# Kernel optimization log

Measured on AMD Instinct MI355X. Metric: run time of the kernel, lower is better.

Reference implementation:

```python
import jax, jax.numpy as jnp
import numpy as np

B, T, E = 64, 64, 256
S, ENC = 128, 1024
RNN, ATT, DENSE = 1024, 1024, 8000


def setup_inputs() -> dict:
    key = jax.random.key(0)
    ks = jax.random.split(key, 16)
    s = 0.02
    return {
        "initial_input": jax.random.normal(ks[0], (B, T, E), jnp.float32),
        "hidden": jax.random.normal(ks[1], (B, RNN), jnp.float32),
        "cell": jax.random.normal(ks[2], (B, RNN), jnp.float32),
        "encoder_output": jax.random.normal(ks[3], (B, S, ENC), jnp.float32),
        "W1": jax.random.normal(ks[4], (RNN, ATT), jnp.float32) * s,
        "b1": jnp.zeros((ATT,), jnp.float32),
        "W2": jax.random.normal(ks[5], (ENC, ATT), jnp.float32) * s,
        "b2": jnp.zeros((ATT,), jnp.float32),
        "V": jax.random.normal(ks[6], (ATT, 1), jnp.float32) * s,
        "bV": jnp.zeros((1,), jnp.float32),
        "kernel": jax.random.normal(ks[7], (ENC + E, 4 * RNN), jnp.float32) * s,
        "rkernel": jax.random.normal(ks[8], (RNN, 4 * RNN), jnp.float32) * s,
        "bias": jnp.zeros((4 * RNN,), jnp.float32),
        "Wd": jax.random.normal(ks[9], (RNN, DENSE), jnp.float32) * s,
        "bd": jnp.zeros((DENSE,), jnp.float32),
        "seq_len": T,
    }


def _decode(initial_input, hidden, cell, encoder_output,
            W1, b1, W2, b2, V, bV, kernel, rkernel, bias, Wd, bd):
    # Keys W2(encoder_output) are step-independent: precompute once. [B,S,ATT]
    keys = jnp.einsum('bse,ea->bsa', encoder_output, W2) + b2

    def step(carry, x_t):
        h, c = carry
        # Bahdanau attention: score = V^T tanh(W1 h + W2 enc)
        q = h @ W1 + b1                                  # [B,ATT]
        score = jnp.tanh(q[:, None, :] + keys) @ V + bV   # [B,S,1]
        attn = jax.nn.softmax(score, axis=1)              # [B,S,1]
        ctx = jnp.sum(attn * encoder_output, axis=1)      # [B,ENC]
        # LSTM cell (Keras gate order i,f,g,o; sigmoid/tanh activations)
        inp = jnp.concatenate([ctx, x_t], axis=-1)        # [B,ENC+E]
        z = inp @ kernel + h @ rkernel + bias              # [B,4*RNN]
        i, f, g, o = jnp.split(z, 4, axis=-1)
        i = jax.nn.sigmoid(i)
        f = jax.nn.sigmoid(f)
        g = jnp.tanh(g)
        o = jax.nn.sigmoid(o)
        c_new = f * c + i * g
        h_new = o * jnp.tanh(c_new)
        logits = h_new @ Wd + bd                           # [B,DENSE]
        return (h_new, c_new), logits

    xs = jnp.swapaxes(initial_input, 0, 1)  # [T,B,E]
    (h, c), logits = jax.lax.scan(step, (hidden, cell), xs)
    outputs = jnp.swapaxes(logits, 0, 1)    # [B,T,DENSE]
    return outputs, h, c


def reference(initial_input, hidden, cell, encoder_output,
              W1, b1, W2, b2, V, bV, kernel, rkernel, bias, Wd, bd, seq_len):
    # seq_len == initial_input.shape[1] (static); the Python loop in the
    # original is expressed as an efficient lax.scan over decode steps.
    return _decode(initial_input[:, :seq_len, :], hidden, cell, encoder_output,
                   W1, b1, W2, b2, V, bV, kernel, rkernel, bias, Wd, bd)
```

## Files before the change

kernel.cpp:

```cpp
#include <hip/hip_runtime.h>
#include <hip/hip_bf16.h>
#include <stdint.h>


typedef __attribute__((ext_vector_type(8))) short short8;
typedef __attribute__((ext_vector_type(4))) float floatx4;
typedef __attribute__((ext_vector_type(4))) unsigned short ushortx4;

__device__ __forceinline__ float b2f(unsigned short u) {
    union { unsigned int i; float f; } v; v.i = ((unsigned int)u) << 16; return v.f;
}
__device__ __forceinline__ unsigned short f2b(float f) {
    union { float f; unsigned int i; } v; v.f = f;
    unsigned int r = v.i + 0x7fffu + ((v.i >> 16) & 1u);
    return (unsigned short)(r >> 16);
}
__device__ __forceinline__ float ftanh(float x) {
    x = fminf(15.f, fmaxf(-15.f, x));
    float e = __expf(2.f * x);
    return (e - 1.f) * __builtin_amdgcn_rcpf(e + 1.f);
}
__device__ __forceinline__ float fsig(float x) {
    return __builtin_amdgcn_rcpf(1.f + __expf(-x));
}
__device__ __forceinline__ void ld_lds16(const void* g, void* l) {
    __builtin_amdgcn_global_load_lds((const __attribute__((address_space(1))) void*)g,
                                     (__attribute__((address_space(3))) void*)l, 16, 0, 0);
}

__global__ __launch_bounds__(256) void conv_f32_bf16(
    const float* __restrict__ src, unsigned short* __restrict__ dst, int n4)
{
    int i = blockIdx.x * 256 + threadIdx.x;
    if (i < n4) {
        float4 v = ((const float4*)src)[i];
        ushortx4 o;
        o[0] = f2b(v.x); o[1] = f2b(v.y); o[2] = f2b(v.z); o[3] = f2b(v.w);
        ((ushortx4*)dst)[i] = o;
    }
}

__global__ __launch_bounds__(256) void transpose_conv(
    const float* __restrict__ src, int srcld,
    unsigned short* __restrict__ dst, int dstld, int coloff, int perm)
{
    __shared__ float tile[32][33];
    const int k0 = blockIdx.y * 32, n0 = blockIdx.x * 32;
    const int r = threadIdx.x >> 3, c = (threadIdx.x & 7) * 4;
    int n = n0 + c;
    int cn = perm ? ((((n >> 4) & 3) << 10) | ((n >> 6) << 4) | (n & 15)) : n;
    float4 v = *(const float4*)&src[(size_t)(k0 + r) * srcld + cn];
    tile[r][c + 0] = v.x; tile[r][c + 1] = v.y;
    tile[r][c + 2] = v.z; tile[r][c + 3] = v.w;
    __syncthreads();
    const int nr = threadIdx.x >> 3, kc = (threadIdx.x & 7) * 4;
    ushortx4 o;
    o[0] = f2b(tile[kc + 0][nr]);
    o[1] = f2b(tile[kc + 1][nr]);
    o[2] = f2b(tile[kc + 2][nr]);
    o[3] = f2b(tile[kc + 3][nr]);
    *(ushortx4*)&dst[(size_t)(n0 + nr) * dstld + coloff + k0 + kc] = o;
}

__global__ __launch_bounds__(256) void gemm_bf16_128(
    const unsigned short* __restrict__ A, int lda,
    const unsigned short* __restrict__ BT, int ldbt, int K,
    float* __restrict__ Cf, unsigned short* __restrict__ Cb,
    int ldc, int ncols, const float* __restrict__ bias)
{
    __shared__ __align__(16) unsigned short As[128 * 32];
    __shared__ __align__(16) unsigned short Bs[128 * 32];
    const int tid = threadIdx.x, wave = tid >> 6, lane = tid & 63;
    const int q = lane >> 4, lm = lane & 15;
    const int wr = wave >> 1, wc = wave & 1;
    const int m0 = blockIdx.y * 128, n0 = blockIdx.x * 128;
    const int srow = lane >> 2;
    const int gch = (lane & 3) ^ ((lane >> 3) & 3);
    const unsigned short* Ag0 = A + (size_t)(m0 + wave * 32 + srow) * lda + gch * 8;
    const unsigned short* Ag1 = Ag0 + (size_t)16 * lda;
    const unsigned short* Bg0 = BT + (size_t)(n0 + wave * 32 + srow) * ldbt + gch * 8;
    const unsigned short* Bg1 = Bg0 + (size_t)16 * ldbt;
    unsigned short* Al0 = &As[(wave * 32) * 32];
    unsigned short* Al1 = &As[(wave * 32 + 16) * 32];
    unsigned short* Bl0 = &Bs[(wave * 32) * 32];
    unsigned short* Bl1 = &Bs[(wave * 32 + 16) * 32];

    const floatx4 z4 = {0.f, 0.f, 0.f, 0.f};
    floatx4 acc[4][4];
#pragma unroll
    for (int i = 0; i < 4; i++)
#pragma unroll
        for (int j = 0; j < 4; j++) acc[i][j] = z4;
    const int ach = ((q ^ ((lm >> 1) & 3))) * 8;

    for (int kb = 0; kb < K; kb += 32) {
        ld_lds16(Ag0 + kb, Al0);
        ld_lds16(Ag1 + kb, Al1);
        ld_lds16(Bg0 + kb, Bl0);
        ld_lds16(Bg1 + kb, Bl1);
        __syncthreads();
        short8 a[4], b[4];
#pragma unroll
        for (int i = 0; i < 4; i++) a[i] = *(const short8*)&As[(wr * 64 + i * 16 + lm) * 32 + ach];
#pragma unroll
        for (int j = 0; j < 4; j++) b[j] = *(const short8*)&Bs[(wc * 64 + j * 16 + lm) * 32 + ach];
#pragma unroll
        for (int i = 0; i < 4; i++)
#pragma unroll
            for (int j = 0; j < 4; j++)
                acc[i][j] = __builtin_amdgcn_mfma_f32_16x16x32_bf16(a[i], b[j], acc[i][j], 0, 0, 0);
        __syncthreads();
    }
    const int rb = m0 + wr * 64 + q * 4;
#pragma unroll
    for (int i = 0; i < 4; i++) {
#pragma unroll
        for (int j = 0; j < 4; j++) {
            int col = n0 + wc * 64 + j * 16 + lm;
            if (col < ncols) {
                float bv = bias ? bias[col] : 0.f;
#pragma unroll
                for (int r = 0; r < 4; r++) {
                    float v = acc[i][j][r] + bv;
                    size_t idx = (size_t)(rb + i * 16 + r) * ldc + col;
                    if (Cf) Cf[idx] = v;
                    if (Cb) Cb[idx] = f2b(v);
                }
            }
        }
    }
}

__global__ __launch_bounds__(256) void gemm64_split(
    const unsigned short* __restrict__ A, int lda,
    const unsigned short* __restrict__ BT, int ldbt,
    int kchunk, float* __restrict__ Cpart, int ldc)
{
    __shared__ __align__(16) unsigned short As[4][64 * 32];
    __shared__ __align__(16) unsigned short Bs[4][64 * 32];
    const int tid = threadIdx.x, wave = tid >> 6, lane = tid & 63;
    const int q = lane >> 4, lm = lane & 15;
    const int n0 = blockIdx.x * 64;
    const int k0 = blockIdx.z * kchunk;
    const int srow = lane >> 2;
    const int gch = (lane & 3) ^ ((lane >> 3) & 3);
    const unsigned short* Ag = A + (size_t)(wave * 16 + srow) * lda + k0 + gch * 8;
    const unsigned short* Bg = BT + (size_t)(n0 + wave * 16 + srow) * ldbt + k0 + gch * 8;
    const int loff = (wave * 16) * 32;
    const floatx4 z4 = {0.f, 0.f, 0.f, 0.f};
    floatx4 acc0 = z4, acc1 = z4, acc2 = z4, acc3 = z4;
    const int ach = ((q ^ ((lm >> 1) & 3))) * 8;
    const int nit = kchunk >> 5;

#pragma unroll
    for (int p = 0; p < 3; ++p) {
        if (p < nit) {
            ld_lds16(Ag + p * 32, &As[p][loff]);
            ld_lds16(Bg + p * 32, &Bs[p][loff]);
        }
    }
    for (int it = 0; it < nit; ++it) {
        const int st = it & 3;
        if (it + 2 < nit)      asm volatile("s_waitcnt vmcnt(4)\n\ts_barrier" ::: "memory");
        else if (it + 1 < nit) asm volatile("s_waitcnt vmcnt(2)\n\ts_barrier" ::: "memory");
        else                   asm volatile("s_waitcnt vmcnt(0)\n\ts_barrier" ::: "memory");
        if (it + 3 < nit) {
            const int sn = (it + 3) & 3;
            ld_lds16(Ag + (it + 3) * 32, &As[sn][loff]);
            ld_lds16(Bg + (it + 3) * 32, &Bs[sn][loff]);
        }
        short8 a  = *(const short8*)&As[st][(wave * 16 + lm) * 32 + ach];
        short8 b0 = *(const short8*)&Bs[st][(0 * 16 + lm) * 32 + ach];
        short8 b1 = *(const short8*)&Bs[st][(1 * 16 + lm) * 32 + ach];
        short8 b2 = *(const short8*)&Bs[st][(2 * 16 + lm) * 32 + ach];
        short8 b3 = *(const short8*)&Bs[st][(3 * 16 + lm) * 32 + ach];
        acc0 = __builtin_amdgcn_mfma_f32_16x16x32_bf16(a, b0, acc0, 0, 0, 0);
        acc1 = __builtin_amdgcn_mfma_f32_16x16x32_bf16(a, b1, acc1, 0, 0, 0);
        acc2 = __builtin_amdgcn_mfma_f32_16x16x32_bf16(a, b2, acc2, 0, 0, 0);
        acc3 = __builtin_amdgcn_mfma_f32_16x16x32_bf16(a, b3, acc3, 0, 0, 0);
    }
    float* Cp = Cpart + (size_t)blockIdx.z * 64 * ldc;
    const int rb = wave * 16 + q * 4;
    floatx4 accs[4] = {acc0, acc1, acc2, acc3};
#pragma unroll
    for (int i = 0; i < 4; i++) {
        int col = n0 + i * 16 + lm;
#pragma unroll
        for (int r = 0; r < 4; r++) Cp[(size_t)(rb + r) * ldc + col] = accs[i][r];
    }
}

__global__ __launch_bounds__(256) void init_hc(
    const float* __restrict__ hidden, const float* __restrict__ cell,
    float* __restrict__ hf, float* __restrict__ cb, unsigned short* __restrict__ hbf)
{
    int idx = blockIdx.x * 256 + threadIdx.x;
    float h = hidden[idx], c = cell[idx];
    hf[idx] = h; cb[idx] = c; hbf[idx] = f2b(h);
}

__global__ __launch_bounds__(256) void attn_scores(
    const float* __restrict__ qp, const float* __restrict__ b1,
    const unsigned short* __restrict__ keys,
    const float* __restrict__ V, const float* __restrict__ bV,
    float* __restrict__ sc)
{
    __shared__ float qs[1024];
    __shared__ float vs[1024];
    const int b = blockIdx.y, sg = blockIdx.x;
    const int tid = threadIdx.x, wave = tid >> 6, lane = tid & 63;
    {
        float4 a0 = ((const float4*)(qp + (size_t)b * 1024))[tid];
        float4 a1 = ((const float4*)(qp + 65536 + (size_t)b * 1024))[tid];
        float4 a2 = ((const float4*)(qp + 131072 + (size_t)b * 1024))[tid];
        float4 a3 = ((const float4*)(qp + 196608 + (size_t)b * 1024))[tid];
        float4 ab = ((const float4*)b1)[tid];
        float4 av = ((const float4*)V)[tid];
        float4 r;
        r.x = a0.x + a1.x + a2.x + a3.x + ab.x;
        r.y = a0.y + a1.y + a2.y + a3.y + ab.y;
        r.z = a0.z + a1.z + a2.z + a3.z + ab.z;
        r.w = a0.w + a1.w + a2.w + a3.w + ab.w;
        *(float4*)&qs[tid * 4] = r;
        *(float4*)&vs[tid * 4] = av;
    }
    __syncthreads();
    float qr[16], vr[16];
#pragma unroll
    for (int i = 0; i < 4; i++) {
        float4 tq = *(const float4*)&qs[lane * 16 + i * 4];
        float4 tv = *(const float4*)&vs[lane * 16 + i * 4];
        qr[i * 4 + 0] = tq.x; qr[i * 4 + 1] = tq.y; qr[i * 4 + 2] = tq.z; qr[i * 4 + 3] = tq.w;
        vr[i * 4 + 0] = tv.x; vr[i * 4 + 1] = tv.y; vr[i * 4 + 2] = tv.z; vr[i * 4 + 3] = tv.w;
    }
    const float bv0 = bV[0];
#pragma unroll
    for (int i = 0; i < 4; i++) {
        const int s = sg * 16 + wave * 4 + i;
        const uint4* kp = (const uint4*)(keys + ((size_t)(b * 128 + s)) * 1024 + lane * 16);
        uint4 k0 = kp[0], k1 = kp[1];
        float kf[16];
        kf[0] = b2f((unsigned short)(k0.x & 0xffff)); kf[1] = b2f((unsigned short)(k0.x >> 16));
        kf[2] = b2f((unsigned short)(k0.y & 0xffff)); kf[3] = b2f((unsigned short)(k0.y >> 16));
        kf[4] = b2f((unsigned short)(k0.z & 0xffff)); kf[5] = b2f((unsigned short)(k0.z >> 16));
        kf[6] = b2f((unsigned short)(k0.w & 0xffff)); kf[7] = b2f((unsigned short)(k0.w >> 16));
        kf[8] = b2f((unsigned short)(k1.x & 0xffff)); kf[9] = b2f((unsigned short)(k1.x >> 16));
        kf[10] = b2f((unsigned short)(k1.y & 0xffff)); kf[11] = b2f((unsigned short)(k1.y >> 16));
        kf[12] = b2f((unsigned short)(k1.z & 0xffff)); kf[13] = b2f((unsigned short)(k1.z >> 16));
        kf[14] = b2f((unsigned short)(k1.w & 0xffff)); kf[15] = b2f((unsigned short)(k1.w >> 16));
        float part = 0.f;
#pragma unroll
        for (int j = 0; j < 16; j++) part += vr[j] * ftanh(qr[j] + kf[j]);
#pragma unroll
        for (int off = 32; off; off >>= 1) part += __shfl_xor(part, off);
        if (lane == 0) sc[b * 128 + s] = part + bv0;
    }
}

__global__ __launch_bounds__(256) void softmax_ctx(
    const float* __restrict__ sc, const unsigned short* __restrict__ enc_bf,
    const float* __restrict__ x, const unsigned short* __restrict__ hbf,
    unsigned short* __restrict__ Axc, int t)
{
    __shared__ float attnv[128];
    __shared__ float red[4][64][2];
    __shared__ float smax_s, ssum_s;
    const int b = blockIdx.y, chunk = blockIdx.x;
    const int tid = threadIdx.x, wave = tid >> 6, lane = tid & 63;
    float sv = 0.f;
    if (tid < 128) { sv = sc[b * 128 + tid]; attnv[tid] = sv; }
    __syncthreads();
    if (tid < 64) {
        float m = fmaxf(attnv[tid], attnv[tid + 64]);
#pragma unroll
        for (int off = 32; off; off >>= 1) m = fmaxf(m, __shfl_xor(m, off));
        if (tid == 0) smax_s = m;
    }
    __syncthreads();
    if (tid < 128) attnv[tid] = __expf(sv - smax_s);
    __syncthreads();
    if (tid < 64) {
        float s2 = attnv[tid] + attnv[tid + 64];
#pragma unroll
        for (int off = 32; off; off >>= 1) s2 += __shfl_xor(s2, off);
        if (tid == 0) ssum_s = s2;
    }
    if (chunk < 2 && tid < 64) {
        int c2 = chunk * 128 + tid * 2;
        float x0 = x[((size_t)b * 64 + t) * 256 + c2];
        float x1 = x[((size_t)b * 64 + t) * 256 + c2 + 1];
        *(unsigned int*)&Axc[b * 2304 + 1024 + c2] =
            (unsigned int)f2b(x0) | ((unsigned int)f2b(x1) << 16);
    }
    if (tid < 64) {
        int c2 = chunk * 128 + tid * 2;
        *(unsigned int*)&Axc[b * 2304 + 1280 + c2] =
            *(const unsigned int*)&hbf[b * 1024 + c2];
    }
    const unsigned int* ep = (const unsigned int*)enc_bf + (size_t)b * 65536 + chunk * 64 + lane;
    __syncthreads();
    float ax = 0.f, ay = 0.f;
#pragma unroll 8
    for (int i = 0; i < 32; i++) {
        int s = wave * 32 + i;
        float a = attnv[s];
        unsigned int u = ep[(size_t)s * 512];
        ax += a * b2f((unsigned short)(u & 0xffff));
        ay += a * b2f((unsigned short)(u >> 16));
    }
    red[wave][lane][0] = ax; red[wave][lane][1] = ay;
    __syncthreads();
    if (tid < 64) {
        float rs = __builtin_amdgcn_rcpf(ssum_s);
        float fx = (red[0][lane][0] + red[1][lane][0] + red[2][lane][0] + red[3][lane][0]) * rs;
        float fy = (red[0][lane][1] + red[1][lane][1] + red[2][lane][1] + red[3][lane][1]) * rs;
        *(unsigned int*)&Axc[b * 2304 + chunk * 128 + lane * 2] =
            (unsigned int)f2b(fx) | ((unsigned int)f2b(fy) << 16);
    }
}

__global__ __launch_bounds__(512) void gemm_gates(
    const unsigned short* __restrict__ Axc,
    const unsigned short* __restrict__ KRT,
    const float* __restrict__ bz,
    float* __restrict__ cb, float* __restrict__ hf,
    unsigned short* __restrict__ hbf, unsigned short* __restrict__ Hall, int t)
{
    __shared__ __align__(16) char smem[65536];
    unsigned short* As = (unsigned short*)smem;
    unsigned short* Bs = (unsigned short*)(smem + 32768);
    float* red = (float*)smem;
    const int tid = threadIdx.x, wave = tid >> 6, lane = tid & 63;
    const int q = lane >> 4, lm = lane & 15;
    const int h = wave >> 2, wm = wave & 3;
    const int bx = blockIdx.x;
    const int srow = lane >> 2;
    const int gch = (lane & 3) ^ ((lane >> 3) & 3);
    const unsigned short* Ag = Axc + (size_t)(wm * 16 + srow) * 2304 + h * 1152 + gch * 8;
    const unsigned short* Bg = KRT + (size_t)(bx * 64 + wm * 16 + srow) * 2304 + h * 1152 + gch * 8;
    const int tileoff = h * 2048;
    const int ldoff = tileoff + (wm * 16) * 32;
    const floatx4 z4 = {0.f, 0.f, 0.f, 0.f};
    floatx4 acc0 = z4, acc1 = z4, acc2 = z4, acc3 = z4;
    const int ach = ((q ^ ((lm >> 1) & 3))) * 8;

#pragma unroll
    for (int p = 0; p < 3; ++p) {
        ld_lds16(Ag + p * 32, &As[p * 4096 + ldoff]);
        ld_lds16(Bg + p * 32, &Bs[p * 4096 + ldoff]);
    }
    for (int it = 0; it < 36; ++it) {
        const int st = it & 3;
        if (it < 34)       asm volatile("s_waitcnt vmcnt(4)\n\ts_barrier" ::: "memory");
        else if (it == 34) asm volatile("s_waitcnt vmcnt(2)\n\ts_barrier" ::: "memory");
        else               asm volatile("s_waitcnt vmcnt(0)\n\ts_barrier" ::: "memory");
        if (it + 3 < 36) {
            const int sn = (it + 3) & 3;
            ld_lds16(Ag + (it + 3) * 32, &As[sn * 4096 + ldoff]);
            ld_lds16(Bg + (it + 3) * 32, &Bs[sn * 4096 + ldoff]);
        }
        const unsigned short* Ast = &As[st * 4096 + tileoff];
        const unsigned short* Bst = &Bs[st * 4096 + tileoff];
        short8 a  = *(const short8*)&Ast[(wm * 16 + lm) * 32 + ach];
        short8 b0 = *(const short8*)&Bst[(0 * 16 + lm) * 32 + ach];
        short8 b1 = *(const short8*)&Bst[(1 * 16 + lm) * 32 + ach];
        short8 b2 = *(const short8*)&Bst[(2 * 16 + lm) * 32 + ach];
        short8 b3 = *(const short8*)&Bst[(3 * 16 + lm) * 32 + ach];
        acc0 = __builtin_amdgcn_mfma_f32_16x16x32_bf16(a, b0, acc0, 0, 0, 0);
        acc1 = __builtin_amdgcn_mfma_f32_16x16x32_bf16(a, b1, acc1, 0, 0, 0);
        acc2 = __builtin_amdgcn_mfma_f32_16x16x32_bf16(a, b2, acc2, 0, 0, 0);
        acc3 = __builtin_amdgcn_mfma_f32_16x16x32_bf16(a, b3, acc3, 0, 0, 0);
    }
    __syncthreads();
    if (h == 1) {
        float* rp = &red[(wm * 64 + lane) * 16];
        *(floatx4*)&rp[0]  = acc0; *(floatx4*)&rp[4]  = acc1;
        *(floatx4*)&rp[8]  = acc2; *(floatx4*)&rp[12] = acc3;
    }
    __syncthreads();
    if (h == 0) {
        const float* rp = &red[(wm * 64 + lane) * 16];
        acc0 += *(const floatx4*)&rp[0];
        acc1 += *(const floatx4*)&rp[4];
        acc2 += *(const floatx4*)&rp[8];
        acc3 += *(const floatx4*)&rp[12];
        const int col = bx * 16 + lm;
        const float bzi = bz[col], bzf = bz[1024 + col];
        const float bzg = bz[2048 + col], bzo = bz[3072 + col];
#pragma unroll
        for (int r = 0; r < 4; ++r) {
            const int b = wm * 16 + q * 4 + r;
            float zi = acc0[r] + bzi;
            float zf = acc1[r] + bzf;
            float zg = acc2[r] + bzg;
            float zo = acc3[r] + bzo;
            float ii = fsig(zi), ff = fsig(zf), gg = ftanh(zg), oo = fsig(zo);
            const int idx = b * 1024 + col;
            float cn = ff * cb[idx] + ii * gg;
            float hn = oo * ftanh(cn);
            cb[idx] = cn; hf[idx] = hn;
            unsigned short hb = f2b(hn);
            hbf[idx] = hb;
            Hall[((size_t)b * 64 + t) * 1024 + col] = hb;
        }
    }
}

__global__ __launch_bounds__(256) void tail_k(
    const float* __restrict__ hf, const float* __restrict__ cb, float* __restrict__ out)
{
    int i = blockIdx.x * 256 + threadIdx.x;
    if (i < 65536) out[32768000 + i] = hf[i];
    else out[32768000 + i] = cb[i - 65536];
}

extern "C" void kernel_launch(void* const* d_in, const int* in_sizes, int n_in,
                              void* d_out, int out_size, void* d_ws, size_t ws_size,
                              hipStream_t stream)
{
    const float* x      = (const float*)d_in[0];
    const float* hidden = (const float*)d_in[1];
    const float* cell   = (const float*)d_in[2];
    const float* enc    = (const float*)d_in[3];
    const float* W1     = (const float*)d_in[4];
    const float* b1     = (const float*)d_in[5];
    const float* W2     = (const float*)d_in[6];
    const float* b2     = (const float*)d_in[7];
    const float* V      = (const float*)d_in[8];
    const float* bV     = (const float*)d_in[9];
    const float* Wk     = (const float*)d_in[10];
    const float* rk     = (const float*)d_in[11];
    const float* bz     = (const float*)d_in[12];
    const float* Wd     = (const float*)d_in[13];
    const float* bd     = (const float*)d_in[14];
    float* out = (float*)d_out;

    char* ws = (char*)d_ws;
    unsigned short* enc_bf  = (unsigned short*)(ws + 0);
    unsigned short* keys_bf = (unsigned short*)(ws + 16777216);
    unsigned short* W1T     = (unsigned short*)(ws + 33554432);
    unsigned short* KRT     = (unsigned short*)(ws + 35651584);
    unsigned short* WdT     = (unsigned short*)(ws + 54525952);
    unsigned short* Hall    = (unsigned short*)(ws + 71041024);
    unsigned short* W2T     = Hall;
    unsigned short* Axc     = (unsigned short*)(ws + 79429632);
    float* qp    = (float*)(ws + 79724544);
    float* scbuf = (float*)(ws + 80773120);
    unsigned short* hbf     = (unsigned short*)(ws + 80805888);
    float* hf    = (float*)(ws + 80936960);
    float* cb    = (float*)(ws + 81199104);

    conv_f32_bf16<<<8192, 256, 0, stream>>>(enc, enc_bf, 8388608 / 4);
    transpose_conv<<<dim3(32, 32),  256, 0, stream>>>(W2, 1024, W2T, 1024, 0, 0);
    transpose_conv<<<dim3(32, 32),  256, 0, stream>>>(W1, 1024, W1T, 1024, 0, 0);
    transpose_conv<<<dim3(128, 32), 256, 0, stream>>>(Wk, 4096, KRT, 2304, 0, 1);
    transpose_conv<<<dim3(128, 8),  256, 0, stream>>>(Wk + 1024 * 4096, 4096, KRT, 2304, 1024, 1);
    transpose_conv<<<dim3(128, 32), 256, 0, stream>>>(rk, 4096, KRT, 2304, 1280, 1);
    transpose_conv<<<dim3(250, 32), 256, 0, stream>>>(Wd, 8000, WdT, 1024, 0, 0);
    init_hc<<<256, 256, 0, stream>>>(hidden, cell, hf, cb, hbf);

    gemm_bf16_128<<<dim3(8, 64), 256, 0, stream>>>(enc_bf, 1024, W2T, 1024, 1024,
                                                   nullptr, keys_bf, 1024, 1024, b2);

    for (int t = 0; t < 64; t++) {
        gemm64_split<<<dim3(16, 1, 4), 256, 0, stream>>>(hbf, 1024, W1T, 1024, 256, qp, 1024);
        attn_scores<<<dim3(8, 64), 256, 0, stream>>>(qp, b1, keys_bf, V, bV, scbuf);
        softmax_ctx<<<dim3(8, 64), 256, 0, stream>>>(scbuf, enc_bf, x, hbf, Axc, t);
        gemm_gates<<<64, 512, 0, stream>>>(Axc, KRT, bz, cb, hf, hbf, Hall, t);
    }

    gemm_bf16_128<<<dim3(63, 32), 256, 0, stream>>>(Hall, 1024, WdT, 1024, 1024,
                                                    out, nullptr, 8000, 8000, bd);
    tail_k<<<512, 256, 0, stream>>>(hf, cb, out);
}
```

Measured before the change: 2.372 ms.

## Fuse per-step decoder kernels into one persistent cooperative kernel with grid syncs

Replaces the 256 per-timestep kernel launches (four kernels per step: query GEMM, attention scores, softmax plus context, gate GEMM) with a single cooperative kernel of 256 blocks that loops over all 64 timesteps and separates phases with grid.sync. The query GEMM is also re-split into 8 K-partials using 512-thread blocks, and the workspace offsets are moved to make room for the larger partial buffer. The aim is to remove launch overhead and inter-kernel gaps on the serial recurrence. In exchange it relies on grid-wide barriers and on all 256 blocks being co-resident, and many blocks sit idle during the GEMM phases.

```diff
diff --git a/kernel.cpp b/kernel.cpp
--- a/kernel.cpp
+++ b/kernel.cpp
@@ -1,4 +1,5 @@
 #include <hip/hip_runtime.h>
+#include <hip/hip_cooperative_groups.h>
 #include <hip/hip_bf16.h>
 #include <stdint.h>
 
@@ -6,6 +7,8 @@
 typedef __attribute__((ext_vector_type(8))) short short8;
 typedef __attribute__((ext_vector_type(4))) float floatx4;
 typedef __attribute__((ext_vector_type(4))) unsigned short ushortx4;
+
+namespace cg = cooperative_groups;
 
 __device__ __forceinline__ float b2f(unsigned short u) {
     union { unsigned int i; float f; } v; v.i = ((unsigned int)u) << 16; return v.f;
@@ -131,65 +134,6 @@
     }
 }
 
-__global__ __launch_bounds__(256) void gemm64_split(
-    const unsigned short* __restrict__ A, int lda,
-    const unsigned short* __restrict__ BT, int ldbt,
-    int kchunk, float* __restrict__ Cpart, int ldc)
-{
-    __shared__ __align__(16) unsigned short As[4][64 * 32];
-    __shared__ __align__(16) unsigned short Bs[4][64 * 32];
-    const int tid = threadIdx.x, wave = tid >> 6, lane = tid & 63;
-    const int q = lane >> 4, lm = lane & 15;
-    const int n0 = blockIdx.x * 64;
-    const int k0 = blockIdx.z * kchunk;
-    const int srow = lane >> 2;
-    const int gch = (lane & 3) ^ ((lane >> 3) & 3);
-    const unsigned short* Ag = A + (size_t)(wave * 16 + srow) * lda + k0 + gch * 8;
-    const unsigned short* Bg = BT + (size_t)(n0 + wave * 16 + srow) * ldbt + k0 + gch * 8;
-    const int loff = (wave * 16) * 32;
-    const floatx4 z4 = {0.f, 0.f, 0.f, 0.f};
-    floatx4 acc0 = z4, acc1 = z4, acc2 = z4, acc3 = z4;
-    const int ach = ((q ^ ((lm >> 1) & 3))) * 8;
-    const int nit = kchunk >> 5;
-
-#pragma unroll
-    for (int p = 0; p < 3; ++p) {
-        if (p < nit) {
-            ld_lds16(Ag + p * 32, &As[p][loff]);
-            ld_lds16(Bg + p * 32, &Bs[p][loff]);
-        }
-    }
-    for (int it = 0; it < nit; ++it) {
-        const int st = it & 3;
-        if (it + 2 < nit)      asm volatile("s_waitcnt vmcnt(4)\n\ts_barrier" ::: "memory");
-        else if (it + 1 < nit) asm volatile("s_waitcnt vmcnt(2)\n\ts_barrier" ::: "memory");
-        else                   asm volatile("s_waitcnt vmcnt(0)\n\ts_barrier" ::: "memory");
-        if (it + 3 < nit) {
-            const int sn = (it + 3) & 3;
-            ld_lds16(Ag + (it + 3) * 32, &As[sn][loff]);
-            ld_lds16(Bg + (it + 3) * 32, &Bs[sn][loff]);
-        }
-        short8 a  = *(const short8*)&As[st][(wave * 16 + lm) * 32 + ach];
-        short8 b0 = *(const short8*)&Bs[st][(0 * 16 + lm) * 32 + ach];
-        short8 b1 = *(const short8*)&Bs[st][(1 * 16 + lm) * 32 + ach];
-        short8 b2 = *(const short8*)&Bs[st][(2 * 16 + lm) * 32 + ach];
-        short8 b3 = *(const short8*)&Bs[st][(3 * 16 + lm) * 32 + ach];
-        acc0 = __builtin_amdgcn_mfma_f32_16x16x32_bf16(a, b0, acc0, 0, 0, 0);
-        acc1 = __builtin_amdgcn_mfma_f32_16x16x32_bf16(a, b1, acc1, 0, 0, 0);
-        acc2 = __builtin_amdgcn_mfma_f32_16x16x32_bf16(a, b2, acc2, 0, 0, 0);
-        acc3 = __builtin_amdgcn_mfma_f32_16x16x32_bf16(a, b3, acc3, 0, 0, 0);
-    }
-    float* Cp = Cpart + (size_t)blockIdx.z * 64 * ldc;
-    const int rb = wave * 16 + q * 4;
-    floatx4 accs[4] = {acc0, acc1, acc2, acc3};
-#pragma unroll
-    for (int i = 0; i < 4; i++) {
-        int col = n0 + i * 16 + lm;
-#pragma unroll
-        for (int r = 0; r < 4; r++) Cp[(size_t)(rb + r) * ldc + col] = accs[i][r];
-    }
-}
-
 __global__ __launch_bounds__(256) void init_hc(
     const float* __restrict__ hidden, const float* __restrict__ cell,
     float* __restrict__ hf, float* __restrict__ cb, unsigned short* __restrict__ hbf)
@@ -199,210 +143,262 @@
     hf[idx] = h; cb[idx] = c; hbf[idx] = f2b(h);
 }
 
-__global__ __launch_bounds__(256) void attn_scores(
-    const float* __restrict__ qp, const float* __restrict__ b1,
-    const unsigned short* __restrict__ keys,
-    const float* __restrict__ V, const float* __restrict__ bV,
-    float* __restrict__ sc)
-{
-    __shared__ float qs[1024];
-    __shared__ float vs[1024];
-    const int b = blockIdx.y, sg = blockIdx.x;
-    const int tid = threadIdx.x, wave = tid >> 6, lane = tid & 63;
-    {
-        float4 a0 = ((const float4*)(qp + (size_t)b * 1024))[tid];
-        float4 a1 = ((const float4*)(qp + 65536 + (size_t)b * 1024))[tid];
-        float4 a2 = ((const float4*)(qp + 131072 + (size_t)b * 1024))[tid];
-        float4 a3 = ((const float4*)(qp + 196608 + (size_t)b * 1024))[tid];
-        float4 ab = ((const float4*)b1)[tid];
-        float4 av = ((const float4*)V)[tid];
-        float4 r;
-        r.x = a0.x + a1.x + a2.x + a3.x + ab.x;
-        r.y = a0.y + a1.y + a2.y + a3.y + ab.y;
-        r.z = a0.z + a1.z + a2.z + a3.z + ab.z;
-        r.w = a0.w + a1.w + a2.w + a3.w + ab.w;
-        *(float4*)&qs[tid * 4] = r;
-        *(float4*)&vs[tid * 4] = av;
-    }
-    __syncthreads();
-    float qr[16], vr[16];
-#pragma unroll
-    for (int i = 0; i < 4; i++) {
-        float4 tq = *(const float4*)&qs[lane * 16 + i * 4];
-        float4 tv = *(const float4*)&vs[lane * 16 + i * 4];
-        qr[i * 4 + 0] = tq.x; qr[i * 4 + 1] = tq.y; qr[i * 4 + 2] = tq.z; qr[i * 4 + 3] = tq.w;
-        vr[i * 4 + 0] = tv.x; vr[i * 4 + 1] = tv.y; vr[i * 4 + 2] = tv.z; vr[i * 4 + 3] = tv.w;
-    }
-    const float bv0 = bV[0];
-#pragma unroll
-    for (int i = 0; i < 4; i++) {
-        const int s = sg * 16 + wave * 4 + i;
-        const uint4* kp = (const uint4*)(keys + ((size_t)(b * 128 + s)) * 1024 + lane * 16);
-        uint4 k0 = kp[0], k1 = kp[1];
-        float kf[16];
-        kf[0] = b2f((unsigned short)(k0.x & 0xffff)); kf[1] = b2f((unsigned short)(k0.x >> 16));
-        kf[2] = b2f((unsigned short)(k0.y & 0xffff)); kf[3] = b2f((unsigned short)(k0.y >> 16));
-        kf[4] = b2f((unsigned short)(k0.z & 0xffff)); kf[5] = b2f((unsigned short)(k0.z >> 16));
-        kf[6] = b2f((unsigned short)(k0.w & 0xffff)); kf[7] = b2f((unsigned short)(k0.w >> 16));
-        kf[8] = b2f((unsigned short)(k1.x & 0xffff)); kf[9] = b2f((unsigned short)(k1.x >> 16));
-        kf[10] = b2f((unsigned short)(k1.y & 0xffff)); kf[11] = b2f((unsigned short)(k1.y >> 16));
-        kf[12] = b2f((unsigned short)(k1.z & 0xffff)); kf[13] = b2f((unsigned short)(k1.z >> 16));
-        kf[14] = b2f((unsigned short)(k1.w & 0xffff)); kf[15] = b2f((unsigned short)(k1.w >> 16));
-        float part = 0.f;
-#pragma unroll
-        for (int j = 0; j < 16; j++) part += vr[j] * ftanh(qr[j] + kf[j]);
-#pragma unroll
-        for (int off = 32; off; off >>= 1) part += __shfl_xor(part, off);
-        if (lane == 0) sc[b * 128 + s] = part + bv0;
-    }
-}
-
-__global__ __launch_bounds__(256) void softmax_ctx(
-    const float* __restrict__ sc, const unsigned short* __restrict__ enc_bf,
-    const float* __restrict__ x, const unsigned short* __restrict__ hbf,
-    unsigned short* __restrict__ Axc, int t)
-{
-    __shared__ float attnv[128];
-    __shared__ float red[4][64][2];
-    __shared__ float smax_s, ssum_s;
-    const int b = blockIdx.y, chunk = blockIdx.x;
-    const int tid = threadIdx.x, wave = tid >> 6, lane = tid & 63;
-    float sv = 0.f;
-    if (tid < 128) { sv = sc[b * 128 + tid]; attnv[tid] = sv; }
-    __syncthreads();
-    if (tid < 64) {
-        float m = fmaxf(attnv[tid], attnv[tid + 64]);
-#pragma unroll
-        for (int off = 32; off; off >>= 1) m = fmaxf(m, __shfl_xor(m, off));
-        if (tid == 0) smax_s = m;
-    }
-    __syncthreads();
-    if (tid < 128) attnv[tid] = __expf(sv - smax_s);
-    __syncthreads();
-    if (tid < 64) {
-        float s2 = attnv[tid] + attnv[tid + 64];
-#pragma unroll
-        for (int off = 32; off; off >>= 1) s2 += __shfl_xor(s2, off);
-        if (tid == 0) ssum_s = s2;
-    }
-    if (chunk < 2 && tid < 64) {
-        int c2 = chunk * 128 + tid * 2;
-        float x0 = x[((size_t)b * 64 + t) * 256 + c2];
-        float x1 = x[((size_t)b * 64 + t) * 256 + c2 + 1];
-        *(unsigned int*)&Axc[b * 2304 + 1024 + c2] =
-            (unsigned int)f2b(x0) | ((unsigned int)f2b(x1) << 16);
-    }
-    if (tid < 64) {
-        int c2 = chunk * 128 + tid * 2;
-        *(unsigned int*)&Axc[b * 2304 + 1280 + c2] =
-            *(const unsigned int*)&hbf[b * 1024 + c2];
-    }
-    const unsigned int* ep = (const unsigned int*)enc_bf + (size_t)b * 65536 + chunk * 64 + lane;
-    __syncthreads();
-    float ax = 0.f, ay = 0.f;
-#pragma unroll 8
-    for (int i = 0; i < 32; i++) {
-        int s = wave * 32 + i;
-        float a = attnv[s];
-        unsigned int u = ep[(size_t)s * 512];
-        ax += a * b2f((unsigned short)(u & 0xffff));
-        ay += a * b2f((unsigned short)(u >> 16));
-    }
-    red[wave][lane][0] = ax; red[wave][lane][1] = ay;
-    __syncthreads();
-    if (tid < 64) {
-        float rs = __builtin_amdgcn_rcpf(ssum_s);
-        float fx = (red[0][lane][0] + red[1][lane][0] + red[2][lane][0] + red[3][lane][0]) * rs;
-        float fy = (red[0][lane][1] + red[1][lane][1] + red[2][lane][1] + red[3][lane][1]) * rs;
-        *(unsigned int*)&Axc[b * 2304 + chunk * 128 + lane * 2] =
-            (unsigned int)f2b(fx) | ((unsigned int)f2b(fy) << 16);
-    }
-}
-
-__global__ __launch_bounds__(512) void gemm_gates(
-    const unsigned short* __restrict__ Axc,
-    const unsigned short* __restrict__ KRT,
-    const float* __restrict__ bz,
-    float* __restrict__ cb, float* __restrict__ hf,
-    unsigned short* __restrict__ hbf, unsigned short* __restrict__ Hall, int t)
-{
+__global__ __launch_bounds__(512) void decoder_k(
+    unsigned short* __restrict__ hbf, const unsigned short* __restrict__ W1T,
+    float* __restrict__ qp, const float* __restrict__ b1,
+    const unsigned short* __restrict__ keys, const float* __restrict__ V,
+    const float* __restrict__ bV, float* __restrict__ sc,
+    const unsigned short* __restrict__ enc_bf, const float* __restrict__ x,
+    unsigned short* __restrict__ Axc, const unsigned short* __restrict__ KRT,
+    const float* __restrict__ bz, float* __restrict__ cb,
+    float* __restrict__ hf, unsigned short* __restrict__ Hall)
+{
+    cg::grid_group grid = cg::this_grid();
     __shared__ __align__(16) char smem[65536];
     unsigned short* As = (unsigned short*)smem;
     unsigned short* Bs = (unsigned short*)(smem + 32768);
-    float* red = (float*)smem;
-    const int tid = threadIdx.x, wave = tid >> 6, lane = tid & 63;
+    const int blk = blockIdx.x, tid = threadIdx.x;
+    const int wave = tid >> 6, lane = tid & 63;
     const int q = lane >> 4, lm = lane & 15;
-    const int h = wave >> 2, wm = wave & 3;
-    const int bx = blockIdx.x;
+    const int wm = wave & 3, h = wave >> 2;
     const int srow = lane >> 2;
     const int gch = (lane & 3) ^ ((lane >> 3) & 3);
-    const unsigned short* Ag = Axc + (size_t)(wm * 16 + srow) * 2304 + h * 1152 + gch * 8;
-    const unsigned short* Bg = KRT + (size_t)(bx * 64 + wm * 16 + srow) * 2304 + h * 1152 + gch * 8;
-    const int tileoff = h * 2048;
-    const int ldoff = tileoff + (wm * 16) * 32;
+    const int ach = ((q ^ ((lm >> 1) & 3))) * 8;
     const floatx4 z4 = {0.f, 0.f, 0.f, 0.f};
-    floatx4 acc0 = z4, acc1 = z4, acc2 = z4, acc3 = z4;
-    const int ach = ((q ^ ((lm >> 1) & 3))) * 8;
-
-#pragma unroll
-    for (int p = 0; p < 3; ++p) {
-        ld_lds16(Ag + p * 32, &As[p * 4096 + ldoff]);
-        ld_lds16(Bg + p * 32, &Bs[p * 4096 + ldoff]);
-    }
-    for (int it = 0; it < 36; ++it) {
-        const int st = it & 3;
-        if (it < 34)       asm volatile("s_waitcnt vmcnt(4)\n\ts_barrier" ::: "memory");
-        else if (it == 34) asm volatile("s_waitcnt vmcnt(2)\n\ts_barrier" ::: "memory");
-        else               asm volatile("s_waitcnt vmcnt(0)\n\ts_barrier" ::: "memory");
-        if (it + 3 < 36) {
-            const int sn = (it + 3) & 3;
-            ld_lds16(Ag + (it + 3) * 32, &As[sn * 4096 + ldoff]);
-            ld_lds16(Bg + (it + 3) * 32, &Bs[sn * 4096 + ldoff]);
+
+    for (int t = 0; t < 64; ++t) {
+        if (blk < 64) {
+            const int bx = blk & 15, kz = blk >> 4;
+            const int k0 = kz * 256 + h * 128;
+            const unsigned short* Ag = hbf + (size_t)(wm * 16 + srow) * 1024 + k0 + gch * 8;
+            const unsigned short* Bg = W1T + (size_t)(bx * 64 + wm * 16 + srow) * 1024 + k0 + gch * 8;
+            const int tileoff = h * 2048;
+            const int ldoff = tileoff + (wm * 16) * 32;
+            floatx4 acc0 = z4, acc1 = z4, acc2 = z4, acc3 = z4;
+#pragma unroll
+            for (int p = 0; p < 3; ++p) {
+                ld_lds16(Ag + p * 32, &As[p * 4096 + ldoff]);
+                ld_lds16(Bg + p * 32, &Bs[p * 4096 + ldoff]);
+            }
+#pragma unroll
+            for (int it = 0; it < 4; ++it) {
+                if (it < 2)       asm volatile("s_waitcnt vmcnt(4)\n\ts_barrier" ::: "memory");
+                else if (it == 2) asm volatile("s_waitcnt vmcnt(2)\n\ts_barrier" ::: "memory");
+                else              asm volatile("s_waitcnt vmcnt(0)\n\ts_barrier" ::: "memory");
+                if (it == 0) {
+                    ld_lds16(Ag + 3 * 32, &As[3 * 4096 + ldoff]);
+                    ld_lds16(Bg + 3 * 32, &Bs[3 * 4096 + ldoff]);
+                }
+                const unsigned short* Ast = &As[it * 4096 + tileoff];
+                const unsigned short* Bst = &Bs[it * 4096 + tileoff];
+                short8 a  = *(const short8*)&Ast[(wm * 16 + lm) * 32 + ach];
+                short8 b0 = *(const short8*)&Bst[(0 * 16 + lm) * 32 + ach];
+                short8 b1v = *(const short8*)&Bst[(1 * 16 + lm) * 32 + ach];
+                short8 b2 = *(const short8*)&Bst[(2 * 16 + lm) * 32 + ach];
+                short8 b3 = *(const short8*)&Bst[(3 * 16 + lm) * 32 + ach];
+                acc0 = __builtin_amdgcn_mfma_f32_16x16x32_bf16(a, b0, acc0, 0, 0, 0);
+                acc1 = __builtin_amdgcn_mfma_f32_16x16x32_bf16(a, b1v, acc1, 0, 0, 0);
+                acc2 = __builtin_amdgcn_mfma_f32_16x16x32_bf16(a, b2, acc2, 0, 0, 0);
+                acc3 = __builtin_amdgcn_mfma_f32_16x16x32_bf16(a, b3, acc3, 0, 0, 0);
+            }
+            float* Q = qp + (size_t)(kz * 2 + h) * 65536;
+            const int rb = wm * 16 + q * 4;
+            floatx4 accs[4] = {acc0, acc1, acc2, acc3};
+#pragma unroll
+            for (int i = 0; i < 4; i++) {
+                int col = bx * 64 + i * 16 + lm;
+#pragma unroll
+                for (int r = 0; r < 4; r++) Q[(size_t)(rb + r) * 1024 + col] = accs[i][r];
+            }
         }
-        const unsigned short* Ast = &As[st * 4096 + tileoff];
-        const unsigned short* Bst = &Bs[st * 4096 + tileoff];
-        short8 a  = *(const short8*)&Ast[(wm * 16 + lm) * 32 + ach];
-        short8 b0 = *(const short8*)&Bst[(0 * 16 + lm) * 32 + ach];
-        short8 b1 = *(const short8*)&Bst[(1 * 16 + lm) * 32 + ach];
-        short8 b2 = *(const short8*)&Bst[(2 * 16 + lm) * 32 + ach];
-        short8 b3 = *(const short8*)&Bst[(3 * 16 + lm) * 32 + ach];
-        acc0 = __builtin_amdgcn_mfma_f32_16x16x32_bf16(a, b0, acc0, 0, 0, 0);
-        acc1 = __builtin_amdgcn_mfma_f32_16x16x32_bf16(a, b1, acc1, 0, 0, 0);
-        acc2 = __builtin_amdgcn_mfma_f32_16x16x32_bf16(a, b2, acc2, 0, 0, 0);
-        acc3 = __builtin_amdgcn_mfma_f32_16x16x32_bf16(a, b3, acc3, 0, 0, 0);
-    }
-    __syncthreads();
-    if (h == 1) {
-        float* rp = &red[(wm * 64 + lane) * 16];
-        *(floatx4*)&rp[0]  = acc0; *(floatx4*)&rp[4]  = acc1;
-        *(floatx4*)&rp[8]  = acc2; *(floatx4*)&rp[12] = acc3;
-    }
-    __syncthreads();
-    if (h == 0) {
-        const float* rp = &red[(wm * 64 + lane) * 16];
-        acc0 += *(const floatx4*)&rp[0];
-        acc1 += *(const floatx4*)&rp[4];
-        acc2 += *(const floatx4*)&rp[8];
-        acc3 += *(const floatx4*)&rp[12];
-        const int col = bx * 16 + lm;
-        const float bzi = bz[col], bzf = bz[1024 + col];
-        const float bzg = bz[2048 + col], bzo = bz[3072 + col];
-#pragma unroll
-        for (int r = 0; r < 4; ++r) {
-            const int b = wm * 16 + q * 4 + r;
-            float zi = acc0[r] + bzi;
-            float zf = acc1[r] + bzf;
-            float zg = acc2[r] + bzg;
-            float zo = acc3[r] + bzo;
-            float ii = fsig(zi), ff = fsig(zf), gg = ftanh(zg), oo = fsig(zo);
-            const int idx = b * 1024 + col;
-            float cn = ff * cb[idx] + ii * gg;
-            float hn = oo * ftanh(cn);
-            cb[idx] = cn; hf[idx] = hn;
-            unsigned short hb = f2b(hn);
-            hbf[idx] = hb;
-            Hall[((size_t)b * 64 + t) * 1024 + col] = hb;
+        grid.sync();
+
+        {
+            const int b = blk >> 2, sg = blk & 3;
+            float* qs = (float*)smem;
+            float* vs = (float*)(smem + 4096);
+            if (tid < 256) {
+                float4 r = ((const float4*)b1)[tid];
+#pragma unroll
+                for (int p = 0; p < 8; ++p) {
+                    float4 a = ((const float4*)(qp + (size_t)p * 65536 + (size_t)b * 1024))[tid];
+                    r.x += a.x; r.y += a.y; r.z += a.z; r.w += a.w;
+                }
+                *(float4*)&qs[tid * 4] = r;
+                *(float4*)&vs[tid * 4] = ((const float4*)V)[tid];
+            }
+            __syncthreads();
+            float qr[16], vr[16];
+#pragma unroll
+            for (int i = 0; i < 4; i++) {
+                float4 tq = *(const float4*)&qs[lane * 16 + i * 4];
+                float4 tv = *(const float4*)&vs[lane * 16 + i * 4];
+                qr[i * 4 + 0] = tq.x; qr[i * 4 + 1] = tq.y; qr[i * 4 + 2] = tq.z; qr[i * 4 + 3] = tq.w;
+                vr[i * 4 + 0] = tv.x; vr[i * 4 + 1] = tv.y; vr[i * 4 + 2] = tv.z; vr[i * 4 + 3] = tv.w;
+            }
+            const float bv0 = bV[0];
+#pragma unroll
+            for (int i = 0; i < 4; i++) {
+                const int s = sg * 32 + wave * 4 + i;
+                const uint4* kp = (const uint4*)(keys + ((size_t)(b * 128 + s)) * 1024 + lane * 16);
+                uint4 k0 = kp[0], k1 = kp[1];
+                float kf[16];
+                kf[0] = b2f((unsigned short)(k0.x & 0xffff)); kf[1] = b2f((unsigned short)(k0.x >> 16));
+                kf[2] = b2f((unsigned short)(k0.y & 0xffff)); kf[3] = b2f((unsigned short)(k0.y >> 16));
+                kf[4] = b2f((unsigned short)(k0.z & 0xffff)); kf[5] = b2f((unsigned short)(k0.z >> 16));
+                kf[6] = b2f((unsigned short)(k0.w & 0xffff)); kf[7] = b2f((unsigned short)(k0.w >> 16));
+                kf[8] = b2f((unsigned short)(k1.x & 0xffff)); kf[9] = b2f((unsigned short)(k1.x >> 16));
+                kf[10] = b2f((unsigned short)(k1.y & 0xffff)); kf[11] = b2f((unsigned short)(k1.y >> 16));
+                kf[12] = b2f((unsigned short)(k1.z & 0xffff)); kf[13] = b2f((unsigned short)(k1.z >> 16));
+                kf[14] = b2f((unsigned short)(k1.w & 0xffff)); kf[15] = b2f((unsigned short)(k1.w >> 16));
+                float part = 0.f;
+#pragma unroll
+                for (int j = 0; j < 16; j++) part += vr[j] * ftanh(qr[j] + kf[j]);
+#pragma unroll
+                for (int off = 32; off; off >>= 1) part += __shfl_xor(part, off);
+                if (lane == 0) sc[b * 128 + s] = part + bv0;
+            }
         }
+        grid.sync();
+
+        {
+            const int b = blk >> 2, q4 = blk & 3;
+            float* attnv = (float*)smem;
+            float* redc  = (float*)(smem + 512);
+            float* misc  = (float*)(smem + 4608);
+            float sv = 0.f;
+            if (tid < 128) { sv = sc[b * 128 + tid]; attnv[tid] = sv; }
+            __syncthreads();
+            if (tid < 64) {
+                float m = fmaxf(attnv[tid], attnv[tid + 64]);
+#pragma unroll
+                for (int off = 32; off; off >>= 1) m = fmaxf(m, __shfl_xor(m, off));
+                if (tid == 0) misc[0] = m;
+            }
+            __syncthreads();
+            if (tid < 128) attnv[tid] = __expf(sv - misc[0]);
+            __syncthreads();
+            if (tid < 64) {
+                float s2 = attnv[tid] + attnv[tid + 64];
+#pragma unroll
+                for (int off = 32; off; off >>= 1) s2 += __shfl_xor(s2, off);
+                if (tid == 0) misc[1] = s2;
+            }
+            if (q4 < 2 && tid < 64) {
+                int c2 = q4 * 128 + tid * 2;
+                float x0 = x[((size_t)b * 64 + t) * 256 + c2];
+                float x1 = x[((size_t)b * 64 + t) * 256 + c2 + 1];
+                *(unsigned int*)&Axc[b * 2304 + 1024 + c2] =
+                    (unsigned int)f2b(x0) | ((unsigned int)f2b(x1) << 16);
+            }
+            if (tid < 128) {
+                int c2 = q4 * 256 + tid * 2;
+                *(unsigned int*)&Axc[b * 2304 + 1280 + c2] =
+                    *(const unsigned int*)&hbf[b * 1024 + c2];
+            }
+            const int cgrp = wave >> 2, sq = wave & 3;
+            const unsigned int* ep = (const unsigned int*)enc_bf + (size_t)b * 65536
+                                     + q4 * 128 + cgrp * 64 + lane;
+            __syncthreads();
+            float ax = 0.f, ay = 0.f;
+#pragma unroll 8
+            for (int i = 0; i < 32; i++) {
+                int s = sq * 32 + i;
+                float a = attnv[s];
+                unsigned int u = ep[(size_t)s * 512];
+                ax += a * b2f((unsigned short)(u & 0xffff));
+                ay += a * b2f((unsigned short)(u >> 16));
+            }
+            redc[((cgrp * 4 + sq) * 64 + lane) * 2]     = ax;
+            redc[((cgrp * 4 + sq) * 64 + lane) * 2 + 1] = ay;
+            __syncthreads();
+            if (tid < 128) {
+                int cg2 = tid >> 6, ln = tid & 63;
+                float rs = __builtin_amdgcn_rcpf(misc[1]);
+                float fx = 0.f, fy = 0.f;
+#pragma unroll
+                for (int s2 = 0; s2 < 4; ++s2) {
+                    fx += redc[((cg2 * 4 + s2) * 64 + ln) * 2];
+                    fy += redc[((cg2 * 4 + s2) * 64 + ln) * 2 + 1];
+                }
+                fx *= rs; fy *= rs;
+                int cu = q4 * 128 + cg2 * 64 + ln;
+                *(unsigned int*)&Axc[b * 2304 + cu * 2] =
+                    (unsigned int)f2b(fx) | ((unsigned int)f2b(fy) << 16);
+            }
+        }
+        grid.sync();
+
+        if (blk < 64) {
+            float* red = (float*)smem;
+            const int bx = blk;
+            const unsigned short* Ag = Axc + (size_t)(wm * 16 + srow) * 2304 + h * 1152 + gch * 8;
+            const unsigned short* Bg = KRT + (size_t)(bx * 64 + wm * 16 + srow) * 2304 + h * 1152 + gch * 8;
+            const int tileoff = h * 2048;
+            const int ldoff = tileoff + (wm * 16) * 32;
+            floatx4 acc0 = z4, acc1 = z4, acc2 = z4, acc3 = z4;
+#pragma unroll
+            for (int p = 0; p < 3; ++p) {
+                ld_lds16(Ag + p * 32, &As[p * 4096 + ldoff]);
+                ld_lds16(Bg + p * 32, &Bs[p * 4096 + ldoff]);
+            }
+            for (int it = 0; it < 36; ++it) {
+                const int st = it & 3;
+                if (it < 34)       asm volatile("s_waitcnt vmcnt(4)\n\ts_barrier" ::: "memory");
+                else if (it == 34) asm volatile("s_waitcnt vmcnt(2)\n\ts_barrier" ::: "memory");
+                else               asm volatile("s_waitcnt vmcnt(0)\n\ts_barrier" ::: "memory");
+                if (it + 3 < 36) {
+                    const int sn = (it + 3) & 3;
+                    ld_lds16(Ag + (it + 3) * 32, &As[sn * 4096 + ldoff]);
+                    ld_lds16(Bg + (it + 3) * 32, &Bs[sn * 4096 + ldoff]);
+                }
+                const unsigned short* Ast = &As[st * 4096 + tileoff];
+                const unsigned short* Bst = &Bs[st * 4096 + tileoff];
+                short8 a  = *(const short8*)&Ast[(wm * 16 + lm) * 32 + ach];
+                short8 b0 = *(const short8*)&Bst[(0 * 16 + lm) * 32 + ach];
+                short8 b1v = *(const short8*)&Bst[(1 * 16 + lm) * 32 + ach];
+                short8 b2 = *(const short8*)&Bst[(2 * 16 + lm) * 32 + ach];
+                short8 b3 = *(const short8*)&Bst[(3 * 16 + lm) * 32 + ach];
+                acc0 = __builtin_amdgcn_mfma_f32_16x16x32_bf16(a, b0, acc0, 0, 0, 0);
+                acc1 = __builtin_amdgcn_mfma_f32_16x16x32_bf16(a, b1v, acc1, 0, 0, 0);
+                acc2 = __builtin_amdgcn_mfma_f32_16x16x32_bf16(a, b2, acc2, 0, 0, 0);
+                acc3 = __builtin_amdgcn_mfma_f32_16x16x32_bf16(a, b3, acc3, 0, 0, 0);
+            }
+            __syncthreads();
+            if (h == 1) {
+                float* rp = &red[(wm * 64 + lane) * 16];
+                *(floatx4*)&rp[0]  = acc0; *(floatx4*)&rp[4]  = acc1;
+                *(floatx4*)&rp[8]  = acc2; *(floatx4*)&rp[12] = acc3;
+            }
+            __syncthreads();
+            if (h == 0) {
+                const float* rp = &red[(wm * 64 + lane) * 16];
+                acc0 += *(const floatx4*)&rp[0];
+                acc1 += *(const floatx4*)&rp[4];
+                acc2 += *(const floatx4*)&rp[8];
+                acc3 += *(const floatx4*)&rp[12];
+                const int col = bx * 16 + lm;
+                const float bzi = bz[col], bzf = bz[1024 + col];
+                const float bzg = bz[2048 + col], bzo = bz[3072 + col];
+#pragma unroll
+                for (int r = 0; r < 4; ++r) {
+                    const int b = wm * 16 + q * 4 + r;
+                    float zi = acc0[r] + bzi;
+                    float zf = acc1[r] + bzf;
+                    float zg = acc2[r] + bzg;
+                    float zo = acc3[r] + bzo;
+                    float ii = fsig(zi), ff = fsig(zf), gg = ftanh(zg), oo = fsig(zo);
+                    const int idx = b * 1024 + col;
+                    float cn = ff * cb[idx] + ii * gg;
+                    float hn = oo * ftanh(cn);
+                    cb[idx] = cn; hf[idx] = hn;
+                    unsigned short hb = f2b(hn);
+                    hbf[idx] = hb;
+                    Hall[((size_t)b * 64 + t) * 1024 + col] = hb;
+                }
+            }
+        }
+        grid.sync();
     }
 }
 
@@ -445,10 +441,10 @@
     unsigned short* W2T     = Hall;
     unsigned short* Axc     = (unsigned short*)(ws + 79429632);
     float* qp    = (float*)(ws + 79724544);
-    float* scbuf = (float*)(ws + 80773120);
-    unsigned short* hbf     = (unsigned short*)(ws + 80805888);
-    float* hf    = (float*)(ws + 80936960);
-    float* cb    = (float*)(ws + 81199104);
+    float* scbuf = (float*)(ws + 81821696);
+    unsigned short* hbf     = (unsigned short*)(ws + 81854464);
+    float* hf    = (float*)(ws + 81985536);
+    float* cb    = (float*)(ws + 82247680);
 
     conv_f32_bf16<<<8192, 256, 0, stream>>>(enc, enc_bf, 8388608 / 4);
     transpose_conv<<<dim3(32, 32),  256, 0, stream>>>(W2, 1024, W2T, 1024, 0, 0);
@@ -462,11 +458,15 @@
     gemm_bf16_128<<<dim3(8, 64), 256, 0, stream>>>(enc_bf, 1024, W2T, 1024, 1024,
                                                    nullptr, keys_bf, 1024, 1024, b2);
 
-    for (int t = 0; t < 64; t++) {
-        gemm64_split<<<dim3(16, 1, 4), 256, 0, stream>>>(hbf, 1024, W1T, 1024, 256, qp, 1024);
-        attn_scores<<<dim3(8, 64), 256, 0, stream>>>(qp, b1, keys_bf, V, bV, scbuf);
-        softmax_ctx<<<dim3(8, 64), 256, 0, stream>>>(scbuf, enc_bf, x, hbf, Axc, t);
-        gemm_gates<<<64, 512, 0, stream>>>(Axc, KRT, bz, cb, hf, hbf, Hall, t);
+    {
+        void* cargs[] = {
+            (void*)&hbf, (void*)&W1T, (void*)&qp, (void*)&b1, (void*)&keys_bf,
+            (void*)&V, (void*)&bV, (void*)&scbuf, (void*)&enc_bf, (void*)&x,
+            (void*)&Axc, (void*)&KRT, (void*)&bz, (void*)&cb, (void*)&hf,
+            (void*)&Hall
+        };
+        hipLaunchCooperativeKernel((void*)decoder_k, dim3(256), dim3(512),
+                                   cargs, 0, stream);
     }
 
     gemm_bf16_128<<<dim3(63, 32), 256, 0, stream>>>(Hall, 1024, WdT, 1024, 1024,
```

Result: slower. 9.050 ms (+281.6%).

## Fuse attention scoring, softmax and context into one per-batch kernel

Applied to the files above, without the earlier changes.

Merges the attention score kernel and the softmax/context kernel into a single kernel with one 512-thread block per batch row. Scores stay in shared memory instead of going through a global buffer, and one kernel launch per decode step is removed. In exchange the grid shrinks from 512 blocks to 64, so each block streams all keys and encoder rows for its batch row serially. This lowers parallelism and memory-level concurrency across the GPU.

```diff
diff --git a/kernel.cpp b/kernel.cpp
--- a/kernel.cpp
+++ b/kernel.cpp
@@ -199,32 +199,40 @@
     hf[idx] = h; cb[idx] = c; hbf[idx] = f2b(h);
 }
 
-__global__ __launch_bounds__(256) void attn_scores(
+__global__ __launch_bounds__(512) void attn_fused(
     const float* __restrict__ qp, const float* __restrict__ b1,
     const unsigned short* __restrict__ keys,
     const float* __restrict__ V, const float* __restrict__ bV,
-    float* __restrict__ sc)
+    const unsigned short* __restrict__ enc_bf, const float* __restrict__ x,
+    const unsigned short* __restrict__ hbf,
+    unsigned short* __restrict__ Axc, int t)
 {
     __shared__ float qs[1024];
     __shared__ float vs[1024];
-    const int b = blockIdx.y, sg = blockIdx.x;
-    const int tid = threadIdx.x, wave = tid >> 6, lane = tid & 63;
-    {
-        float4 a0 = ((const float4*)(qp + (size_t)b * 1024))[tid];
-        float4 a1 = ((const float4*)(qp + 65536 + (size_t)b * 1024))[tid];
-        float4 a2 = ((const float4*)(qp + 131072 + (size_t)b * 1024))[tid];
-        float4 a3 = ((const float4*)(qp + 196608 + (size_t)b * 1024))[tid];
-        float4 ab = ((const float4*)b1)[tid];
-        float4 av = ((const float4*)V)[tid];
-        float4 r;
-        r.x = a0.x + a1.x + a2.x + a3.x + ab.x;
-        r.y = a0.y + a1.y + a2.y + a3.y + ab.y;
-        r.z = a0.z + a1.z + a2.z + a3.z + ab.z;
-        r.w = a0.w + a1.w + a2.w + a3.w + ab.w;
+    __shared__ float attnv[128];
+    __shared__ float misc[2];
+    const int b = blockIdx.x, tid = threadIdx.x;
+    const int wave = tid >> 6, lane = tid & 63;
+
+    if (tid < 256) {
+        float4 r = ((const float4*)b1)[tid];
+#pragma unroll
+        for (int p = 0; p < 4; ++p) {
+            float4 a = ((const float4*)(qp + (size_t)p * 65536 + (size_t)b * 1024))[tid];
+            r.x += a.x; r.y += a.y; r.z += a.z; r.w += a.w;
+        }
         *(float4*)&qs[tid * 4] = r;
-        *(float4*)&vs[tid * 4] = av;
-    }
-    __syncthreads();
+        *(float4*)&vs[tid * 4] = ((const float4*)V)[tid];
+    }
+    if (tid < 128) {
+        float x0 = x[((size_t)b * 64 + t) * 256 + tid * 2];
+        float x1 = x[((size_t)b * 64 + t) * 256 + tid * 2 + 1];
+        ((unsigned int*)&Axc[b * 2304 + 1024])[tid] =
+            (unsigned int)f2b(x0) | ((unsigned int)f2b(x1) << 16);
+    }
+    ((unsigned int*)&Axc[b * 2304 + 1280])[tid] = ((const unsigned int*)&hbf[b * 1024])[tid];
+    __syncthreads();
+
     float qr[16], vr[16];
 #pragma unroll
     for (int i = 0; i < 4; i++) {
@@ -234,9 +242,9 @@
         vr[i * 4 + 0] = tv.x; vr[i * 4 + 1] = tv.y; vr[i * 4 + 2] = tv.z; vr[i * 4 + 3] = tv.w;
     }
     const float bv0 = bV[0];
-#pragma unroll
-    for (int i = 0; i < 4; i++) {
-        const int s = sg * 16 + wave * 4 + i;
+#pragma unroll 2
+    for (int i = 0; i < 16; i++) {
+        const int s = wave * 16 + i;
         const uint4* kp = (const uint4*)(keys + ((size_t)(b * 128 + s)) * 1024 + lane * 16);
         uint4 k0 = kp[0], k1 = kp[1];
         float kf[16];
@@ -253,70 +261,35 @@
         for (int j = 0; j < 16; j++) part += vr[j] * ftanh(qr[j] + kf[j]);
 #pragma unroll
         for (int off = 32; off; off >>= 1) part += __shfl_xor(part, off);
-        if (lane == 0) sc[b * 128 + s] = part + bv0;
-    }
-}
-
-__global__ __launch_bounds__(256) void softmax_ctx(
-    const float* __restrict__ sc, const unsigned short* __restrict__ enc_bf,
-    const float* __restrict__ x, const unsigned short* __restrict__ hbf,
-    unsigned short* __restrict__ Axc, int t)
-{
-    __shared__ float attnv[128];
-    __shared__ float red[4][64][2];
-    __shared__ float smax_s, ssum_s;
-    const int b = blockIdx.y, chunk = blockIdx.x;
-    const int tid = threadIdx.x, wave = tid >> 6, lane = tid & 63;
-    float sv = 0.f;
-    if (tid < 128) { sv = sc[b * 128 + tid]; attnv[tid] = sv; }
+        if (lane == 0) attnv[s] = part + bv0;
+    }
     __syncthreads();
     if (tid < 64) {
-        float m = fmaxf(attnv[tid], attnv[tid + 64]);
+        float a0 = attnv[tid], a1 = attnv[tid + 64];
+        float m = fmaxf(a0, a1);
 #pragma unroll
         for (int off = 32; off; off >>= 1) m = fmaxf(m, __shfl_xor(m, off));
-        if (tid == 0) smax_s = m;
-    }
-    __syncthreads();
-    if (tid < 128) attnv[tid] = __expf(sv - smax_s);
-    __syncthreads();
-    if (tid < 64) {
-        float s2 = attnv[tid] + attnv[tid + 64];
+        float e0 = __expf(a0 - m), e1 = __expf(a1 - m);
+        attnv[tid] = e0; attnv[tid + 64] = e1;
+        float s2 = e0 + e1;
 #pragma unroll
         for (int off = 32; off; off >>= 1) s2 += __shfl_xor(s2, off);
-        if (tid == 0) ssum_s = s2;
-    }
-    if (chunk < 2 && tid < 64) {
-        int c2 = chunk * 128 + tid * 2;
-        float x0 = x[((size_t)b * 64 + t) * 256 + c2];
-        float x1 = x[((size_t)b * 64 + t) * 256 + c2 + 1];
-        *(unsigned int*)&Axc[b * 2304 + 1024 + c2] =
-            (unsigned int)f2b(x0) | ((unsigned int)f2b(x1) << 16);
-    }
-    if (tid < 64) {
-        int c2 = chunk * 128 + tid * 2;
-        *(unsigned int*)&Axc[b * 2304 + 1280 + c2] =
-            *(const unsigned int*)&hbf[b * 1024 + c2];
-    }
-    const unsigned int* ep = (const unsigned int*)enc_bf + (size_t)b * 65536 + chunk * 64 + lane;
-    __syncthreads();
+        if (tid == 0) misc[0] = s2;
+    }
+    __syncthreads();
+    const float rs = __builtin_amdgcn_rcpf(misc[0]);
+    const unsigned int* ep = (const unsigned int*)enc_bf + (size_t)b * 65536 + tid;
     float ax = 0.f, ay = 0.f;
 #pragma unroll 8
-    for (int i = 0; i < 32; i++) {
-        int s = wave * 32 + i;
+    for (int s = 0; s < 128; s++) {
         float a = attnv[s];
         unsigned int u = ep[(size_t)s * 512];
         ax += a * b2f((unsigned short)(u & 0xffff));
         ay += a * b2f((unsigned short)(u >> 16));
     }
-    red[wave][lane][0] = ax; red[wave][lane][1] = ay;
-    __syncthreads();
-    if (tid < 64) {
-        float rs = __builtin_amdgcn_rcpf(ssum_s);
-        float fx = (red[0][lane][0] + red[1][lane][0] + red[2][lane][0] + red[3][lane][0]) * rs;
-        float fy = (red[0][lane][1] + red[1][lane][1] + red[2][lane][1] + red[3][lane][1]) * rs;
-        *(unsigned int*)&Axc[b * 2304 + chunk * 128 + lane * 2] =
-            (unsigned int)f2b(fx) | ((unsigned int)f2b(fy) << 16);
-    }
+    ax *= rs; ay *= rs;
+    ((unsigned int*)&Axc[b * 2304])[tid] =
+        (unsigned int)f2b(ax) | ((unsigned int)f2b(ay) << 16);
 }
 
 __global__ __launch_bounds__(512) void gemm_gates(
@@ -445,10 +418,9 @@
     unsigned short* W2T     = Hall;
     unsigned short* Axc     = (unsigned short*)(ws + 79429632);
     float* qp    = (float*)(ws + 79724544);
-    float* scbuf = (float*)(ws + 80773120);
-    unsigned short* hbf     = (unsigned short*)(ws + 80805888);
-    float* hf    = (float*)(ws + 80936960);
-    float* cb    = (float*)(ws + 81199104);
+    unsigned short* hbf     = (unsigned short*)(ws + 80773120);
+    float* hf    = (float*)(ws + 80904192);
+    float* cb    = (float*)(ws + 81166336);
 
     conv_f32_bf16<<<8192, 256, 0, stream>>>(enc, enc_bf, 8388608 / 4);
     transpose_conv<<<dim3(32, 32),  256, 0, stream>>>(W2, 1024, W2T, 1024, 0, 0);
@@ -464,8 +436,7 @@
 
     for (int t = 0; t < 64; t++) {
         gemm64_split<<<dim3(16, 1, 4), 256, 0, stream>>>(hbf, 1024, W1T, 1024, 256, qp, 1024);
-        attn_scores<<<dim3(8, 64), 256, 0, stream>>>(qp, b1, keys_bf, V, bV, scbuf);
-        softmax_ctx<<<dim3(8, 64), 256, 0, stream>>>(scbuf, enc_bf, x, hbf, Axc, t);
+        attn_fused<<<64, 512, 0, stream>>>(qp, b1, keys_bf, V, bV, enc_bf, x, hbf, Axc, t);
         gemm_gates<<<64, 512, 0, stream>>>(Axc, KRT, bz, cb, hf, hbf, Hall, t);
     }
 
```

Result: slower. 3.366 ms (+41.9%).
